# Kernel tuning notes

Measured on AMD Instinct MI355X. Metric: run time of the kernel, lower is better.

## Reference

```python
import jax, jax.numpy as jnp
import numpy as np

B, TIN, IN, TRI, D, FFN, L, OUT = 8, 1040, 80, 128, 512, 2048, 8, 1024
H, DH, STRIDE, SEG, RC, LC, MAXMEM = 8, 64, 4, 16, 4, 32, 4
NEG = -1e8
SCALE = DH ** -0.5


def _layer_norm(x, g, b, eps=1e-5):
    m = jnp.mean(x, -1, keepdims=True)
    v = jnp.var(x, -1, keepdims=True)
    return (x - m) * jax.lax.rsqrt(v + eps) * g + b


def _build_attention_mask(U, nseg):
    # Faithful port of Emformer._gen_attention_mask; True = masked out.
    rct = RC * nseg
    mlen = nseg - 1
    rc_rows, q_rows, s_rows = [], [], []
    for i in range(nseg):
        rs, re = i * RC, i * RC + RC
        ss, se = max(i * SEG - LC, 0), min((i + 1) * SEG, U)
        ms = max(i - MAXMEM, 0)
        widths = [ms, i - ms, mlen - i, rs, RC, rct - re, ss, se - ss, U - se]

        def row(allowed):
            return np.concatenate([np.full(max(w, 0), j in allowed, dtype=bool)
                                   for j, w in enumerate(widths)])

        r = row({1, 4, 7})  # memory, own rc block, own (left-extended) segment
        rc_rows.append(np.tile(r, (RC, 1)))
        q_rows.append(np.tile(r, (min(SEG, U - i * SEG), 1)))
        s_rows.append(row({4, 7})[None])  # summary: rc block + segment only
    allow = np.concatenate([np.concatenate(rc_rows), np.concatenate(q_rows), np.concatenate(s_rows)])
    return jnp.asarray(~allow)


def _forward(input, lengths, w_in, ln_in_g, ln_in_b, wq, bq, wk, bk, wv, bv, wo, bo,
             ff_ln_g, ff_ln_b, w1, b1, w2, b2, ln_out_g, ln_out_b, w_out, b_out, lng, lnb):
    x = input @ w_in                                    # (B, TIN, TRI) input_linear (no bias)
    nb, t, _ = x.shape
    nf = t - t % STRIDE
    x = x[:, :nf].reshape(nb, nf // STRIDE, TRI * STRIDE)  # time reduction -> (B, Tr, D)
    lr = lengths // STRIDE
    x = jnp.transpose(x, (1, 0, 2))                     # (Tr, B, D) time-major like torch Emformer
    Tr = x.shape[0]
    U = Tr - RC                                         # utterance length (256)
    nseg = -(-U // SEG)
    utt = x[:U]
    # right-context blocks: hard-copied per segment (last block = trailing rc)
    starts = np.concatenate([np.arange(1, nseg) * SEG, [Tr - RC]])
    idx = (starts[:, None] + np.arange(RC)[None, :]).reshape(-1)
    rc = x[idx]                                         # (nseg*RC, B, D)
    Rt = rc.shape[0]
    Q = Rt + U + nseg                                   # rc + utterance + summary queries
    K = (nseg - 1) + Rt + U                             # mems + rc + utterance keys
    attn_mask = _build_attention_mask(U, nseg)          # (Q, K)
    mems0 = utt.reshape(nseg, SEG, nb, D).mean(1)[:-1]  # AvgPool1d(seg) on raw utterance, drop last
    # padding mask over keys (faithful to _gen_padding_mask)
    rcbl = Q - jnp.max(lr) - nseg
    klen = lr + (nseg - 1) + rcbl
    pad = jnp.arange(K)[None, :] >= klen[:, None]       # (B, K), True = masked

    def step(carry, p):
        utt, rc, mems = carry
        g1, be1, Wq, Bq, Wk, Bk, Wv, Bv, Wo, Bo, g2, be2, Wf1, Bf1, Wf2, Bf2, g3, be3 = p
        ln = _layer_norm(jnp.concatenate([rc, utt]), g1, be1)
        ln_rc, ln_utt = ln[:Rt], ln[Rt:]
        summary = ln_utt.reshape(nseg, SEG, nb, D).mean(1)       # (nseg, B, D)
        qin = jnp.concatenate([ln_rc, ln_utt, summary])          # (Q, B, D)
        kin = jnp.concatenate([mems, ln_rc, ln_utt])             # (K, B, D)
        q = (qin @ Wq + Bq).reshape(Q, nb, H, DH)
        k = (kin @ Wk + Bk).reshape(K, nb, H, DH)
        v = (kin @ Wv + Bv).reshape(K, nb, H, DH)
        w = jnp.einsum('qbhd,kbhd->bhqk', q * SCALE, k)
        w = jnp.where(attn_mask[None, None], NEG, w)
        w = jnp.where(pad[:, None, None, :], NEG, w)
        probs = jax.nn.softmax(w, axis=-1)
        att = jnp.einsum('bhqk,kbhd->qbhd', probs, v).reshape(Q, nb, D)
        out = att @ Wo + Bo
        rcu = out[:Rt + U]
        new_mems = jnp.tanh(out[Rt + U:])[:-1]                   # tanh_on_mem=True, drop last summary
        res = rcu + jnp.concatenate([rc, utt])                   # residual w/ pre-LN input
        h = _layer_norm(res, g2, be2)
        h = jax.nn.relu(h @ Wf1 + Bf1) @ Wf2 + Bf2               # pos_ff (pre-LN inside)
        res = res + h
        res = _layer_norm(res, g3, be3)
        return (res[Rt:], res[:Rt], new_mems), None

    xs = (ln_in_g, ln_in_b, wq, bq, wk, bk, wv, bv, wo, bo,
          ff_ln_g, ff_ln_b, w1, b1, w2, b2, ln_out_g, ln_out_b)
    (utt, rc, mems), _ = jax.lax.scan(step, (utt, rc, mems0), xs)
    y = jnp.transpose(utt, (1, 0, 2))                   # (B, U, D)
    y = _layer_norm(y @ w_out + b_out, lng, lnb)        # output_linear + LayerNorm
    return y, lr


def setup_inputs() -> dict:
    key = jax.random.key(0)
    ks = jax.random.split(key, 12)

    def w(k, shape, fan):
        return jax.random.normal(k, shape, jnp.float32) / np.sqrt(fan)

    return {
        "input": jax.random.normal(ks[0], (B, TIN, IN), jnp.float32),
        "lengths": jax.random.randint(ks[1], (B,), 256, 1025, jnp.int32),
        "w_in": w(ks[2], (IN, TRI), IN),
        "ln_in_g": jnp.ones((L, D), jnp.float32), "ln_in_b": jnp.zeros((L, D), jnp.float32),
        "wq": w(ks[3], (L, D, D), D), "bq": jnp.zeros((L, D), jnp.float32),
        "wk": w(ks[4], (L, D, D), D), "bk": jnp.zeros((L, D), jnp.float32),
        "wv": w(ks[5], (L, D, D), D), "bv": jnp.zeros((L, D), jnp.float32),
        "wo": w(ks[6], (L, D, D), D), "bo": jnp.zeros((L, D), jnp.float32),
        "ff_ln_g": jnp.ones((L, D), jnp.float32), "ff_ln_b": jnp.zeros((L, D), jnp.float32),
        "w1": w(ks[7], (L, D, FFN), D), "b1": jnp.zeros((L, FFN), jnp.float32),
        "w2": w(ks[8], (L, FFN, D), FFN), "b2": jnp.zeros((L, D), jnp.float32),
        "ln_out_g": jnp.ones((L, D), jnp.float32), "ln_out_b": jnp.zeros((L, D), jnp.float32),
        "w_out": w(ks[9], (D, OUT), D), "b_out": jnp.zeros((OUT,), jnp.float32),
        "lng": jnp.ones((OUT,), jnp.float32), "lnb": jnp.zeros((OUT,), jnp.float32),
    }


def reference(input, lengths, w_in, ln_in_g, ln_in_b, wq, bq, wk, bk, wv, bv, wo, bo,
              ff_ln_g, ff_ln_b, w1, b1, w2, b2, ln_out_g, ln_out_b, w_out, b_out, lng, lnb):
    return _forward(input, lengths, w_in, ln_in_g, ln_in_b, wq, bq, wk, bk, wv, bv, wo, bo,
                    ff_ln_g, ff_ln_b, w1, b1, w2, b2, ln_out_g, ln_out_b, w_out, b_out, lng, lnb)
```

## Files before the change

kernel.cpp:

```cpp
#include <hip/hip_runtime.h>
#include <math.h>

#define NB 8
#define D 512
#define H 8
#define DH 64
#define NSEG 16
#define RT 64
#define UU 256
#define QN 336
#define KN 335
#define SROWS 320
#define FFN_D 2048
#define LAYERS 8
#define OUTD 1024
#define TR 260
#define NEGV (-100000000.0f)
#define QSCALE 0.125f

typedef __attribute__((ext_vector_type(8))) short bf16x8;
typedef __attribute__((ext_vector_type(4))) float f32x4;

__device__ inline unsigned short f2bf(float f) {
    union { float f; unsigned int u; } v; v.f = f;
    unsigned int u = v.u;
    unsigned int r = (u + 0x7FFFu + ((u >> 16) & 1u)) >> 16;
    return (unsigned short)r;
}
__device__ inline float bf2f(unsigned short h) {
    union { unsigned int u; float f; } v; v.u = ((unsigned int)h) << 16;
    return v.f;
}

__device__ inline void async16(const void* g, void* l) {
    __builtin_amdgcn_global_load_lds((const __attribute__((address_space(1))) void*)g,
                                     (__attribute__((address_space(3))) void*)l, 16, 0, 0);
}

__global__ void lr_k(const int* __restrict__ lengths, int* __restrict__ lrw,
                     float* __restrict__ out_lr) {
    if (threadIdx.x == 0) {
        int mx = 0;
        for (int b = 0; b < NB; ++b) {
            int v = lengths[b] >> 2;
            lrw[b] = v;
            out_lr[b] = (float)v;
            if (v > mx) mx = v;
        }
        lrw[NB] = mx;
    }
}

__global__ __launch_bounds__(128) void inproj_k(const float* __restrict__ input,
                                                const float* __restrict__ w_in,
                                                float* __restrict__ XB) {
    __shared__ float wl[80 * 128];
    __shared__ float il[4 * 80];
    int tid = threadIdx.x;
    int t = blockIdx.x >> 3;
    int b = blockIdx.x & 7;
    for (int i = tid; i < 80 * 128; i += 128) wl[i] = w_in[i];
    const float* inp = input + ((size_t)b * 1040 + (size_t)t * 4) * 80;
    for (int i = tid; i < 320; i += 128) il[i] = inp[i];
    __syncthreads();
    float* xrow = XB + ((size_t)(t * NB + b)) * D;
#pragma unroll
    for (int c = 0; c < 4; ++c) {
        float acc = 0.f;
        for (int i = 0; i < 80; ++i) acc = fmaf(il[c * 80 + i], wl[i * 128 + tid], acc);
        xrow[c * 128 + tid] = acc;
    }
}

__global__ __launch_bounds__(256) void initstate_k(const float* __restrict__ XB,
                                                   float* __restrict__ S) {
    int r = blockIdx.x;
    int srow = r >> 3, b = r & 7;
    int src;
    if (srow < RT) {
        int i = srow >> 2, jj = srow & 3;
        src = (i < 15 ? (i + 1) * 16 : 256) + jj;
    } else {
        src = srow - RT;
    }
    const float* xr = XB + ((size_t)(src * NB + b)) * D;
    float* sr = S + (size_t)r * D;
    sr[threadIdx.x] = xr[threadIdx.x];
    sr[threadIdx.x + 256] = xr[threadIdx.x + 256];
}

__global__ __launch_bounds__(256) void mems0_k(const float* __restrict__ XB,
                                               unsigned short* __restrict__ MEMS) {
    int ib = blockIdx.x;
    int i = ib >> 3, b = ib & 7;
    for (int c = 0; c < 2; ++c) {
        int col = threadIdx.x + c * 256;
        float s = 0.f;
#pragma unroll
        for (int t = 0; t < 16; ++t) s += XB[((size_t)((i * 16 + t) * NB + b)) * D + col];
        MEMS[(size_t)ib * D + col] = f2bf(s * (1.f / 16.f));
    }
}

__global__ __launch_bounds__(256) void ln2_k(float* __restrict__ X,
                                             unsigned short* __restrict__ Y16,
                                             const float* __restrict__ gA,
                                             const float* __restrict__ bA,
                                             const float* __restrict__ gB,
                                             const float* __restrict__ bB, int fused) {
    int row = blockIdx.x;
    float* x = X + (size_t)row * D;
    __shared__ float rs_[4], rss_[4], rs2[4], rss2[4];
    int w = threadIdx.x >> 6;
    float v[2];
    float s = 0.f, ss = 0.f;
#pragma unroll
    for (int j = 0; j < 2; ++j) {
        v[j] = x[threadIdx.x + j * 256];
        s += v[j];
        ss = fmaf(v[j], v[j], ss);
    }
#pragma unroll
    for (int off = 32; off; off >>= 1) {
        s += __shfl_xor(s, off);
        ss += __shfl_xor(ss, off);
    }
    if ((threadIdx.x & 63) == 0) { rs_[w] = s; rss_[w] = ss; }
    __syncthreads();
    s = rs_[0] + rs_[1] + rs_[2] + rs_[3];
    ss = rss_[0] + rss_[1] + rss_[2] + rss_[3];
    float mean = s * (1.f / D);
    float var = ss * (1.f / D) - mean * mean;
    float rstd = rsqrtf(var + 1e-5f);
    float y1[2];
#pragma unroll
    for (int j = 0; j < 2; ++j) {
        int col = threadIdx.x + j * 256;
        y1[j] = (v[j] - mean) * rstd * gA[col] + bA[col];
    }
    if (!fused) {
#pragma unroll
        for (int j = 0; j < 2; ++j)
            Y16[(size_t)row * D + threadIdx.x + j * 256] = f2bf(y1[j]);
        return;
    }
    float s2 = 0.f, ss2 = 0.f;
#pragma unroll
    for (int j = 0; j < 2; ++j) {
        s2 += y1[j];
        ss2 = fmaf(y1[j], y1[j], ss2);
    }
#pragma unroll
    for (int off = 32; off; off >>= 1) {
        s2 += __shfl_xor(s2, off);
        ss2 += __shfl_xor(ss2, off);
    }
    if ((threadIdx.x & 63) == 0) { rs2[w] = s2; rss2[w] = ss2; }
    __syncthreads();
    s2 = rs2[0] + rs2[1] + rs2[2] + rs2[3];
    ss2 = rss2[0] + rss2[1] + rss2[2] + rss2[3];
    float mean2 = s2 * (1.f / D);
    float var2 = ss2 * (1.f / D) - mean2 * mean2;
    float rstd2 = rsqrtf(var2 + 1e-5f);
#pragma unroll
    for (int j = 0; j < 2; ++j) {
        int col = threadIdx.x + j * 256;
        x[col] = y1[j];
        Y16[(size_t)row * D + col] = f2bf((y1[j] - mean2) * rstd2 * gB[col] + bB[col]);
    }
}

__global__ __launch_bounds__(256) void ln_res_k(const float* __restrict__ OUTB,
                                                float* __restrict__ SB,
                                                unsigned short* __restrict__ MEMS,
                                                unsigned short* __restrict__ Y16,
                                                const float* __restrict__ g,
                                                const float* __restrict__ be) {
    int row = blockIdx.x;
    if (row >= SROWS * NB) {
        int j = row - SROWS * NB;
#pragma unroll
        for (int c = 0; c < 2; ++c) {
            int col = threadIdx.x + c * 256;
            MEMS[(size_t)j * D + col] = f2bf(tanhf(OUTB[(size_t)row * D + col]));
        }
        return;
    }
    float v[2];
    float s = 0.f, ss = 0.f;
#pragma unroll
    for (int j = 0; j < 2; ++j) {
        int col = threadIdx.x + j * 256;
        float r = SB[(size_t)row * D + col] + OUTB[(size_t)row * D + col];
        SB[(size_t)row * D + col] = r;
        v[j] = r;
        s += r;
        ss = fmaf(r, r, ss);
    }
#pragma unroll
    for (int off = 32; off; off >>= 1) {
        s += __shfl_xor(s, off);
        ss += __shfl_xor(ss, off);
    }
    __shared__ float rs_[4], rss_[4];
    int w = threadIdx.x >> 6;
    if ((threadIdx.x & 63) == 0) {
        rs_[w] = s;
        rss_[w] = ss;
    }
    __syncthreads();
    s = rs_[0] + rs_[1] + rs_[2] + rs_[3];
    ss = rss_[0] + rss_[1] + rss_[2] + rss_[3];
    float mean = s * (1.f / D);
    float var = ss * (1.f / D) - mean * mean;
    float rstd = rsqrtf(var + 1e-5f);
#pragma unroll
    for (int j = 0; j < 2; ++j) {
        int col = threadIdx.x + j * 256;
        Y16[(size_t)row * D + col] = f2bf((v[j] - mean) * rstd * g[col] + be[col]);
    }
}

__global__ __launch_bounds__(256) void summary_k(const unsigned short* __restrict__ LN16,
                                                 unsigned short* __restrict__ SUM16) {
    int ib = blockIdx.x;
    int i = ib >> 3, b = ib & 7;
    for (int c = 0; c < 2; ++c) {
        int col = threadIdx.x + c * 256;
        float s = 0.f;
#pragma unroll
        for (int t = 0; t < 16; ++t)
            s += bf2f(LN16[((size_t)((RT + i * 16 + t) * NB + b)) * D + col]);
        SUM16[(size_t)ib * D + col] = f2bf(s * (1.f / 16.f));
    }
}

__device__ inline void conv_tile64(float (*tile)[65], const float* __restrict__ src, int srcN,
                                   int k0, int sn0, unsigned short* __restrict__ dst, int dstK,
                                   int dn0) {
    int t = threadIdx.x;
#pragma unroll
    for (int p = 0; p < 4; ++p) {
        int r = p * 16 + (t >> 4);
        int c = (t & 15) * 4;
        *(float4*)&tile[r][c] = *(const float4*)&src[(size_t)(k0 + r) * srcN + sn0 + c];
    }
    __syncthreads();
#pragma unroll
    for (int p = 0; p < 2; ++p) {
        int rn = p * 32 + (t >> 3);
        int kc = (t & 7) * 8;
        int4 o;
        o.x = (int)f2bf(tile[kc + 0][rn]) | ((int)f2bf(tile[kc + 1][rn]) << 16);
        o.y = (int)f2bf(tile[kc + 2][rn]) | ((int)f2bf(tile[kc + 3][rn]) << 16);
        o.z = (int)f2bf(tile[kc + 4][rn]) | ((int)f2bf(tile[kc + 5][rn]) << 16);
        o.w = (int)f2bf(tile[kc + 6][rn]) | ((int)f2bf(tile[kc + 7][rn]) << 16);
        *(int4*)&dst[(size_t)(dn0 + rn) * dstK + k0 + kc] = o;
    }
    __syncthreads();
}

__global__ __launch_bounds__(256) void convw_all_k(const float* __restrict__ wq,
                                                   const float* __restrict__ wk,
                                                   const float* __restrict__ wv,
                                                   const float* __restrict__ wo,
                                                   const float* __restrict__ w1,
                                                   const float* __restrict__ w2,
                                                   const float* __restrict__ bq,
                                                   const float* __restrict__ bk,
                                                   const float* __restrict__ bv,
                                                   const float* __restrict__ w_out,
                                                   unsigned short* __restrict__ WQKV,
                                                   unsigned short* __restrict__ WO16,
                                                   unsigned short* __restrict__ W1T,
                                                   unsigned short* __restrict__ W2T,
                                                   unsigned short* __restrict__ WOUT16,
                                                   float* __restrict__ BQKV) {
    __shared__ float tile[64][65];
    int tb = blockIdx.x;
    if (tb >= LAYERS * 768) {
        int t = tb - LAYERS * 768;
        int n0 = (t % 16) * 64, k0 = (t / 16) * 64;
        conv_tile64(tile, w_out, 1024, k0, n0, WOUT16, 512, n0);
        return;
    }
    int l = tb / 768, t = tb % 768;
    if (t == 0) {
        for (int i = threadIdx.x; i < 1536; i += 256)
            BQKV[l * 1536 + i] = i < 512 ? bq[l * 512 + i]
                                         : (i < 1024 ? bk[l * 512 + i - 512]
                                                     : bv[l * 512 + i - 1024]);
    }
    if (t < 192) {
        int n0 = (t % 24) * 64, k0 = (t / 24) * 64;
        const float* src;
        int sn0;
        if (n0 < 512) { src = wq + (size_t)l * 262144; sn0 = n0; }
        else if (n0 < 1024) { src = wk + (size_t)l * 262144; sn0 = n0 - 512; }
        else { src = wv + (size_t)l * 262144; sn0 = n0 - 1024; }
        conv_tile64(tile, src, 512, k0, sn0, WQKV + (size_t)l * 1536 * 512, 512, n0);
    } else if (t < 256) {
        int tt = t - 192;
        int n0 = (tt % 8) * 64, k0 = (tt / 8) * 64;
        conv_tile64(tile, wo + (size_t)l * 262144, 512, k0, n0, WO16 + (size_t)l * 512 * 512, 512,
                    n0);
    } else if (t < 512) {
        int tt = t - 256;
        int n0 = (tt % 32) * 64, k0 = (tt / 32) * 64;
        conv_tile64(tile, w1 + (size_t)l * 1048576, 2048, k0, n0, W1T + (size_t)l * 2048 * 512,
                    512, n0);
    } else {
        int tt = t - 512;
        int n0 = (tt % 8) * 64, k0 = (tt / 8) * 64;
        conv_tile64(tile, w2 + (size_t)l * 1048576, 512, k0, n0, W2T + (size_t)l * 512 * 2048,
                    2048, n0);
    }
}

template <int BK>
__global__ __launch_bounds__(256) void gemm16_k(const unsigned short* __restrict__ A,
                                                const unsigned short* __restrict__ BT,
                                                const float* __restrict__ bias,
                                                void* __restrict__ Cp, int M, int N, int K,
                                                int Kchunk, int flags) {
    constexpr int CH = BK / 8;
    constexpr int NQ = CH / 4;
    __shared__ unsigned short As[64 * BK];
    __shared__ unsigned short Bs[64 * BK];
    int tid = threadIdx.x;
    int wave = tid >> 6, lane = tid & 63;
    int wm = wave >> 1, wn = wave & 1;
    int quad = lane >> 4, sub = lane & 15;
    int m0 = blockIdx.y * 64, n0 = blockIdx.x * 64;
    int kb = blockIdx.z * Kchunk;

    const unsigned short* gA[NQ];
    const unsigned short* gB[NQ];
    unsigned short* lA[NQ];
    unsigned short* lB[NQ];
#pragma unroll
    for (int q = 0; q < NQ; ++q) {
        int s = wave * (64 * NQ) + q * 64 + lane;
        int r = s / CH;
        int c = (s % CH) ^ (r & (CH - 1));
        int gra = m0 + r;
        if (gra >= M) gra = M - 1;
        gA[q] = A + (size_t)gra * K + kb + c * 8;
        gB[q] = BT + (size_t)(n0 + r) * K + kb + c * 8;
        lA[q] = &As[(wave * (64 * NQ) + q * 64) * 8];
        lB[q] = &Bs[(wave * (64 * NQ) + q * 64) * 8];
    }

    int rowA0 = wm * 32 + sub, rowA1 = rowA0 + 16;
    int rowB0 = wn * 32 + sub, rowB1 = rowB0 + 16;

    f32x4 acc[2][2] = {};
    for (int k0 = 0; k0 < Kchunk; k0 += BK) {
#pragma unroll
        for (int q = 0; q < NQ; ++q) {
            async16(gA[q] + k0, lA[q]);
            async16(gB[q] + k0, lB[q]);
        }
        __syncthreads();
#pragma unroll
        for (int ks = 0; ks < BK / 32; ++ks) {
            int cc = ks * 4 + quad;
            bf16x8 af0 = *(const bf16x8*)&As[rowA0 * BK + ((cc ^ (rowA0 & (CH - 1))) * 8)];
            bf16x8 af1 = *(const bf16x8*)&As[rowA1 * BK + ((cc ^ (rowA1 & (CH - 1))) * 8)];
            bf16x8 bf0 = *(const bf16x8*)&Bs[rowB0 * BK + ((cc ^ (rowB0 & (CH - 1))) * 8)];
            bf16x8 bf1 = *(const bf16x8*)&Bs[rowB1 * BK + ((cc ^ (rowB1 & (CH - 1))) * 8)];
            acc[0][0] = __builtin_amdgcn_mfma_f32_16x16x32_bf16(af0, bf0, acc[0][0], 0, 0, 0);
            acc[0][1] = __builtin_amdgcn_mfma_f32_16x16x32_bf16(af0, bf1, acc[0][1], 0, 0, 0);
            acc[1][0] = __builtin_amdgcn_mfma_f32_16x16x32_bf16(af1, bf0, acc[1][0], 0, 0, 0);
            acc[1][1] = __builtin_amdgcn_mfma_f32_16x16x32_bf16(af1, bf1, acc[1][1], 0, 0, 0);
        }
        __syncthreads();
    }

    bool relu = flags & 1, addc = flags & 2, obf = flags & 4, atom = flags & 8;
    bool addbias = !atom || blockIdx.z == 0;
    float* Cf = (float*)Cp;
    unsigned short* Ch = (unsigned short*)Cp;
#pragma unroll
    for (int mi = 0; mi < 2; ++mi) {
#pragma unroll
        for (int ni = 0; ni < 2; ++ni) {
#pragma unroll
            for (int r = 0; r < 4; ++r) {
                int row = m0 + wm * 32 + mi * 16 + quad * 4 + r;
                int col = n0 + wn * 32 + ni * 16 + sub;
                if (row < M) {
                    float v = acc[mi][ni][r] + (addbias ? bias[col] : 0.f);
                    if (relu) v = fmaxf(v, 0.f);
                    size_t idx = (size_t)row * N + col;
                    if (obf) {
                        Ch[idx] = f2bf(v);
                    } else if (atom) {
                        atomicAdd(&Cf[idx], v);
                    } else {
                        if (addc) v += Cf[idx];
                        Cf[idx] = v;
                    }
                }
            }
        }
    }
}

__global__ __launch_bounds__(256) void attn_k(const unsigned short* __restrict__ QKV,
                                              unsigned short* __restrict__ ATT,
                                              const int* __restrict__ lrw) {
    int tid = threadIdx.x;
    int qrow = blockIdx.x;
    int b = blockIdx.y;

    int i, is_sum;
    if (qrow < RT) {
        i = qrow >> 2;
        is_sum = 0;
    } else if (qrow < RT + UU) {
        i = (qrow - RT) >> 4;
        is_sum = 0;
    } else {
        i = qrow - (RT + UU);
        is_sum = 1;
    }
    int ms = (i > 4) ? (i - 4) : 0;
    int n_mem = is_sum ? 0 : (i - ms);
    int us = (i * 16 - 32 > 0) ? (i * 16 - 32) : 0;
    int ue = (i + 1) * 16;
    int total = n_mem + 4 + (ue - us);
    int klen = KN + lrw[b] - lrw[NB];

    __shared__ float qs[512];
    __shared__ float sc[H][64];
    __shared__ int kks[64];

    {
        const unsigned int* qrp =
            (const unsigned int*)&QKV[(size_t)(120 + qrow * NB + b) * 1536];
        unsigned int u = qrp[tid];
        qs[2 * tid] = __uint_as_float(u << 16) * QSCALE;
        qs[2 * tid + 1] = __uint_as_float(u & 0xFFFF0000u) * QSCALE;
    }
    if (tid < 64) {
        int kk = -1;
        if (tid < total) {
            if (tid < n_mem)
                kk = ms + tid;
            else if (tid < n_mem + 4)
                kk = 15 + i * 4 + (tid - n_mem);
            else
                kk = 79 + us + (tid - n_mem - 4);
        }
        kks[tid] = kk;
    }
    __syncthreads();

#pragma unroll
    for (int rep = 0; rep < 2; ++rep) {
        int p = rep * 256 + tid;
        int h = p >> 6, j = p & 63;
        int kk = kks[j];
        float s = NEGV;
        if (kk >= 0 && kk < klen) {
            const int4* kr = (const int4*)&QKV[(size_t)(kk * NB + b) * 1536 + 512 + h * DH];
            const float* qh = &qs[h * DH];
            float accd = 0.f;
#pragma unroll
            for (int c = 0; c < 8; ++c) {
                int4 kv = kr[c];
                const int uu[4] = {kv.x, kv.y, kv.z, kv.w};
#pragma unroll
                for (int jj = 0; jj < 4; ++jj) {
                    float lo = __uint_as_float(((unsigned)uu[jj]) << 16);
                    float hi = __uint_as_float(((unsigned)uu[jj]) & 0xFFFF0000u);
                    accd = fmaf(lo, qh[c * 8 + jj * 2], accd);
                    accd = fmaf(hi, qh[c * 8 + jj * 2 + 1], accd);
                }
            }
            s = accd;
        }
        sc[h][j] = s;
    }
    __syncthreads();

    {
        int wv = tid >> 6, lane = tid & 63;
#pragma unroll
        for (int hh = 0; hh < 2; ++hh) {
            int h = wv + hh * 4;
            float s = sc[h][lane];
            float m = s;
#pragma unroll
            for (int off = 32; off; off >>= 1) m = fmaxf(m, __shfl_xor(m, off));
            float p = __expf(s - m);
            float sum = p;
#pragma unroll
            for (int off = 32; off; off >>= 1) sum += __shfl_xor(sum, off);
            sc[h][lane] = p / sum;
        }
    }
    __syncthreads();

    {
        int h = tid >> 5;
        const float* ph = sc[h];
        float a0 = 0.f, a1 = 0.f;
        const unsigned short* vbase = QKV + (size_t)b * 1536 + 1024 + 2 * tid;
#pragma unroll 4
        for (int j = 0; j < total; ++j) {
            int kkj = kks[j];
            unsigned int u = *(const unsigned int*)&vbase[(size_t)kkj * (NB * 1536)];
            float p = ph[j];
            a0 = fmaf(p, __uint_as_float(u << 16), a0);
            a1 = fmaf(p, __uint_as_float(u & 0xFFFF0000u), a1);
        }
        unsigned int o = ((unsigned int)f2bf(a0)) | (((unsigned int)f2bf(a1)) << 16);
        *(unsigned int*)&ATT[(size_t)(qrow * NB + b) * D + 2 * tid] = o;
    }
}

__global__ __launch_bounds__(256) void final_ln_k(const float* __restrict__ Yb,
                                                  const float* __restrict__ g,
                                                  const float* __restrict__ be,
                                                  float* __restrict__ out) {
    int row = blockIdx.x;
    int u = row >> 3, b = row & 7;
    const float* x = Yb + (size_t)row * OUTD;
    float v[4];
    float s = 0.f, ss = 0.f;
#pragma unroll
    for (int j = 0; j < 4; ++j) {
        v[j] = x[threadIdx.x + j * 256];
        s += v[j];
        ss = fmaf(v[j], v[j], ss);
    }
#pragma unroll
    for (int off = 32; off; off >>= 1) {
        s += __shfl_xor(s, off);
        ss += __shfl_xor(ss, off);
    }
    __shared__ float rs_[4], rss_[4];
    int w = threadIdx.x >> 6;
    if ((threadIdx.x & 63) == 0) {
        rs_[w] = s;
        rss_[w] = ss;
    }
    __syncthreads();
    s = rs_[0] + rs_[1] + rs_[2] + rs_[3];
    ss = rss_[0] + rss_[1] + rss_[2] + rss_[3];
    float mean = s * (1.f / OUTD);
    float var = ss * (1.f / OUTD) - mean * mean;
    float rstd = rsqrtf(var + 1e-5f);
    float* o = out + ((size_t)(b * 256 + u)) * OUTD;
#pragma unroll
    for (int j = 0; j < 4; ++j) {
        int col = threadIdx.x + j * 256;
        o[col] = (v[j] - mean) * rstd * g[col] + be[col];
    }
}

extern "C" void kernel_launch(void* const* d_in, const int* in_sizes, int n_in, void* d_out,
                              int out_size, void* d_ws, size_t ws_size, hipStream_t stream) {
    (void)in_sizes;
    (void)n_in;
    (void)out_size;
    (void)ws_size;
    const float* input = (const float*)d_in[0];
    const int* lengths = (const int*)d_in[1];
    const float* w_in = (const float*)d_in[2];
    const float* ln_in_g = (const float*)d_in[3];
    const float* ln_in_b = (const float*)d_in[4];
    const float* wq = (const float*)d_in[5];
    const float* bq = (const float*)d_in[6];
    const float* wk = (const float*)d_in[7];
    const float* bk = (const float*)d_in[8];
    const float* wv = (const float*)d_in[9];
    const float* bv = (const float*)d_in[10];
    const float* wo = (const float*)d_in[11];
    const float* bo = (const float*)d_in[12];
    const float* ff_g = (const float*)d_in[13];
    const float* ff_b = (const float*)d_in[14];
    const float* w1 = (const float*)d_in[15];
    const float* b1 = (const float*)d_in[16];
    const float* w2 = (const float*)d_in[17];
    const float* b2 = (const float*)d_in[18];
    const float* lo_g = (const float*)d_in[19];
    const float* lo_b = (const float*)d_in[20];
    const float* w_out = (const float*)d_in[21];
    const float* b_out = (const float*)d_in[22];
    const float* lng = (const float*)d_in[23];
    const float* lnb = (const float*)d_in[24];
    float* out = (float*)d_out;

    char* wsc = (char*)d_ws;
    size_t off = 0;
    auto alloc = [&](size_t bytes) {
        char* p = wsc + off;
        off += (bytes + 255) & ~(size_t)255;
        return p;
    };
    unsigned short* ACT16 = (unsigned short*)alloc(2816ULL * 512 * 2);
    unsigned short* ATT16 = (unsigned short*)alloc(2688ULL * 512 * 2);
    unsigned short* HB16 = (unsigned short*)alloc(2560ULL * 2048 * 2);
    unsigned short* QKVB = (unsigned short*)alloc(2816ULL * 1536 * 2);
    float* SB = (float*)alloc(2560ULL * 512 * 4);
    unsigned short* WQKV16 = (unsigned short*)alloc(8ULL * 1536 * 512 * 2);
    unsigned short* WO16 = (unsigned short*)alloc(8ULL * 512 * 512 * 2);
    unsigned short* W1T = (unsigned short*)alloc(8ULL * 2048 * 512 * 2);
    unsigned short* W2T = (unsigned short*)alloc(8ULL * 512 * 2048 * 2);
    unsigned short* WOUT16 = (unsigned short*)alloc(1024ULL * 512 * 2);
    float* BQKV = (float*)alloc(8ULL * 1536 * 4);
    int* LRW = (int*)alloc(64);

    unsigned short* MEMS16 = ACT16;
    unsigned short* LNB16 = ACT16 + 120 * 512;
    unsigned short* SUMB16 = ACT16 + 2680 * 512;
    float* XB = (float*)QKVB;
    float* OUTB = (float*)QKVB;
    float* HBf = (float*)QKVB;

    lr_k<<<1, 64, 0, stream>>>(lengths, LRW, out + (size_t)NB * 256 * 1024);
    convw_all_k<<<LAYERS * 768 + 128, 256, 0, stream>>>(wq, wk, wv, wo, w1, w2, bq, bk, bv,
                                                        w_out, WQKV16, WO16, W1T, W2T, WOUT16,
                                                        BQKV);
    inproj_k<<<TR * NB, 128, 0, stream>>>(input, w_in, XB);
    initstate_k<<<SROWS * NB, 256, 0, stream>>>(XB, SB);
    mems0_k<<<15 * NB, 256, 0, stream>>>(XB, MEMS16);

    for (int l = 0; l < LAYERS; ++l) {
        if (l == 0) {
            ln2_k<<<SROWS * NB, 256, 0, stream>>>(SB, LNB16, ln_in_g, ln_in_b, nullptr, nullptr,
                                                  0);
        } else {
            ln2_k<<<SROWS * NB, 256, 0, stream>>>(SB, LNB16, lo_g + (l - 1) * D,
                                                  lo_b + (l - 1) * D, ln_in_g + l * D,
                                                  ln_in_b + l * D, 1);
        }
        summary_k<<<NSEG * NB, 256, 0, stream>>>(LNB16, SUMB16);
        gemm16_k<128><<<dim3(24, 44, 1), 256, 0, stream>>>(
            ACT16, WQKV16 + (size_t)l * 1536 * 512, BQKV + l * 1536, QKVB, 2808, 1536, 512, 512,
            4);
        attn_k<<<dim3(QN, NB), 256, 0, stream>>>(QKVB, ATT16, LRW);
        gemm16_k<128><<<dim3(8, 42, 1), 256, 0, stream>>>(ATT16, WO16 + (size_t)l * 512 * 512,
                                                          bo + l * D, OUTB, QN * NB, D, D, 512,
                                                          0);
        ln_res_k<<<(SROWS + 15) * NB, 256, 0, stream>>>(OUTB, SB, MEMS16, LNB16, ff_g + l * D,
                                                        ff_b + l * D);
        gemm16_k<128><<<dim3(32, 40, 1), 256, 0, stream>>>(LNB16, W1T + (size_t)l * 2048 * 512,
                                                           b1 + l * FFN_D, HB16, SROWS * NB,
                                                           FFN_D, 512, 512, 1 | 4);
        gemm16_k<128><<<dim3(8, 40, 4), 256, 0, stream>>>(HB16, W2T + (size_t)l * 512 * 2048,
                                                          b2 + l * D, SB, SROWS * NB, D, FFN_D,
                                                          512, 8);
    }
    ln2_k<<<SROWS * NB, 256, 0, stream>>>(SB, LNB16, lo_g + 7 * D, lo_b + 7 * D, nullptr,
                                          nullptr, 0);
    gemm16_k<128><<<dim3(16, 32, 1), 256, 0, stream>>>(LNB16 + (size_t)RT * NB * D, WOUT16,
                                                       b_out, HBf, UU * NB, OUTD, 512, 512, 0);
    final_ln_k<<<UU * NB, 256, 0, stream>>>(HBf, lng, lnb, out);
}
```

Before: 1.170 ms.

## Double-buffer GEMM K-tiles and fold summary query into attention via linearity

The GEMM kernel now uses BK=64 with two LDS buffers, issuing async loads for the next K-tile while computing on the current one. This removes one barrier per iteration and overlaps global loads with MFMA work. Separately, the summary_k kernel is dropped. The summary query is computed inside attention as the mean of the projected queries of its 16 segment rows, which relies on the Q projection being linear. That shrinks the QKV GEMM by 128 rows and removes a launch, but the summary K/V rows it used to project are no longer computed, and rounding order changes slightly.

```diff
diff --git a/kernel.cpp b/kernel.cpp
--- a/kernel.cpp
+++ b/kernel.cpp
@@ -218,20 +218,6 @@
     for (int j = 0; j < 2; ++j) {
         int col = threadIdx.x + j * 256;
         Y16[(size_t)row * D + col] = f2bf((v[j] - mean) * rstd * g[col] + be[col]);
-    }
-}
-
-__global__ __launch_bounds__(256) void summary_k(const unsigned short* __restrict__ LN16,
-                                                 unsigned short* __restrict__ SUM16) {
-    int ib = blockIdx.x;
-    int i = ib >> 3, b = ib & 7;
-    for (int c = 0; c < 2; ++c) {
-        int col = threadIdx.x + c * 256;
-        float s = 0.f;
-#pragma unroll
-        for (int t = 0; t < 16; ++t)
-            s += bf2f(LN16[((size_t)((RT + i * 16 + t) * NB + b)) * D + col]);
-        SUM16[(size_t)ib * D + col] = f2bf(s * (1.f / 16.f));
     }
 }
 
@@ -317,16 +303,13 @@
     }
 }
 
-template <int BK>
 __global__ __launch_bounds__(256) void gemm16_k(const unsigned short* __restrict__ A,
                                                 const unsigned short* __restrict__ BT,
                                                 const float* __restrict__ bias,
                                                 void* __restrict__ Cp, int M, int N, int K,
                                                 int Kchunk, int flags) {
-    constexpr int CH = BK / 8;
-    constexpr int NQ = CH / 4;
-    __shared__ unsigned short As[64 * BK];
-    __shared__ unsigned short Bs[64 * BK];
+    __shared__ unsigned short As[2 * 64 * 64];
+    __shared__ unsigned short Bs[2 * 64 * 64];
     int tid = threadIdx.x;
     int wave = tid >> 6, lane = tid & 63;
     int wm = wave >> 1, wn = wave & 1;
@@ -334,47 +317,53 @@
     int m0 = blockIdx.y * 64, n0 = blockIdx.x * 64;
     int kb = blockIdx.z * Kchunk;
 
-    const unsigned short* gA[NQ];
-    const unsigned short* gB[NQ];
-    unsigned short* lA[NQ];
-    unsigned short* lB[NQ];
-#pragma unroll
-    for (int q = 0; q < NQ; ++q) {
-        int s = wave * (64 * NQ) + q * 64 + lane;
-        int r = s / CH;
-        int c = (s % CH) ^ (r & (CH - 1));
-        int gra = m0 + r;
-        if (gra >= M) gra = M - 1;
-        gA[q] = A + (size_t)gra * K + kb + c * 8;
-        gB[q] = BT + (size_t)(n0 + r) * K + kb + c * 8;
-        lA[q] = &As[(wave * (64 * NQ) + q * 64) * 8];
-        lB[q] = &Bs[(wave * (64 * NQ) + q * 64) * 8];
-    }
+    int s0 = wave * 128 + lane;
+    int s1 = s0 + 64;
+    int r0 = s0 >> 3, c0 = (s0 & 7) ^ (r0 & 7);
+    int r1 = s1 >> 3, c1 = (s1 & 7) ^ (r1 & 7);
+    int gra0 = m0 + r0; if (gra0 >= M) gra0 = M - 1;
+    int gra1 = m0 + r1; if (gra1 >= M) gra1 = M - 1;
+    const unsigned short* gA0 = A + (size_t)gra0 * K + kb + c0 * 8;
+    const unsigned short* gA1 = A + (size_t)gra1 * K + kb + c1 * 8;
+    const unsigned short* gB0 = BT + (size_t)(n0 + r0) * K + kb + c0 * 8;
+    const unsigned short* gB1 = BT + (size_t)(n0 + r1) * K + kb + c1 * 8;
+    int lo0 = (wave * 128) * 8;
+    int lo1 = (wave * 128 + 64) * 8;
 
     int rowA0 = wm * 32 + sub, rowA1 = rowA0 + 16;
     int rowB0 = wn * 32 + sub, rowB1 = rowB0 + 16;
 
+    int nIter = Kchunk >> 6;
     f32x4 acc[2][2] = {};
-    for (int k0 = 0; k0 < Kchunk; k0 += BK) {
-#pragma unroll
-        for (int q = 0; q < NQ; ++q) {
-            async16(gA[q] + k0, lA[q]);
-            async16(gB[q] + k0, lB[q]);
-        }
+
+    async16(gA0, &As[lo0]);
+    async16(gA1, &As[lo1]);
+    async16(gB0, &Bs[lo0]);
+    async16(gB1, &Bs[lo1]);
+
+    for (int it = 0; it < nIter; ++it) {
         __syncthreads();
-#pragma unroll
-        for (int ks = 0; ks < BK / 32; ++ks) {
+        int bo = (it & 1) * 4096;
+        if (it + 1 < nIter) {
+            int nb = ((it + 1) & 1) * 4096;
+            int ko = (it + 1) * 64;
+            async16(gA0 + ko, &As[nb + lo0]);
+            async16(gA1 + ko, &As[nb + lo1]);
+            async16(gB0 + ko, &Bs[nb + lo0]);
+            async16(gB1 + ko, &Bs[nb + lo1]);
+        }
+#pragma unroll
+        for (int ks = 0; ks < 2; ++ks) {
             int cc = ks * 4 + quad;
-            bf16x8 af0 = *(const bf16x8*)&As[rowA0 * BK + ((cc ^ (rowA0 & (CH - 1))) * 8)];
-            bf16x8 af1 = *(const bf16x8*)&As[rowA1 * BK + ((cc ^ (rowA1 & (CH - 1))) * 8)];
-            bf16x8 bf0 = *(const bf16x8*)&Bs[rowB0 * BK + ((cc ^ (rowB0 & (CH - 1))) * 8)];
-            bf16x8 bf1 = *(const bf16x8*)&Bs[rowB1 * BK + ((cc ^ (rowB1 & (CH - 1))) * 8)];
+            bf16x8 af0 = *(const bf16x8*)&As[bo + rowA0 * 64 + ((cc ^ (rowA0 & 7)) * 8)];
+            bf16x8 af1 = *(const bf16x8*)&As[bo + rowA1 * 64 + ((cc ^ (rowA1 & 7)) * 8)];
+            bf16x8 bf0 = *(const bf16x8*)&Bs[bo + rowB0 * 64 + ((cc ^ (rowB0 & 7)) * 8)];
+            bf16x8 bf1 = *(const bf16x8*)&Bs[bo + rowB1 * 64 + ((cc ^ (rowB1 & 7)) * 8)];
             acc[0][0] = __builtin_amdgcn_mfma_f32_16x16x32_bf16(af0, bf0, acc[0][0], 0, 0, 0);
             acc[0][1] = __builtin_amdgcn_mfma_f32_16x16x32_bf16(af0, bf1, acc[0][1], 0, 0, 0);
             acc[1][0] = __builtin_amdgcn_mfma_f32_16x16x32_bf16(af1, bf0, acc[1][0], 0, 0, 0);
             acc[1][1] = __builtin_amdgcn_mfma_f32_16x16x32_bf16(af1, bf1, acc[1][1], 0, 0, 0);
         }
-        __syncthreads();
     }
 
     bool relu = flags & 1, addc = flags & 2, obf = flags & 4, atom = flags & 8;
@@ -436,12 +425,24 @@
     __shared__ float sc[H][64];
     __shared__ int kks[64];
 
-    {
+    if (!is_sum) {
         const unsigned int* qrp =
             (const unsigned int*)&QKV[(size_t)(120 + qrow * NB + b) * 1536];
         unsigned int u = qrp[tid];
         qs[2 * tid] = __uint_as_float(u << 16) * QSCALE;
         qs[2 * tid + 1] = __uint_as_float(u & 0xFFFF0000u) * QSCALE;
+    } else {
+        const unsigned int* qrp =
+            (const unsigned int*)&QKV[(size_t)(120 + (RT + i * 16) * NB + b) * 1536];
+        float a0 = 0.f, a1 = 0.f;
+#pragma unroll
+        for (int t = 0; t < 16; ++t) {
+            unsigned int u = qrp[(size_t)t * (NB * 768) + tid];
+            a0 += __uint_as_float(u << 16);
+            a1 += __uint_as_float(u & 0xFFFF0000u);
+        }
+        qs[2 * tid] = a0 * (QSCALE / 16.f);
+        qs[2 * tid + 1] = a1 * (QSCALE / 16.f);
     }
     if (tid < 64) {
         int kk = -1;
@@ -601,10 +602,10 @@
         off += (bytes + 255) & ~(size_t)255;
         return p;
     };
-    unsigned short* ACT16 = (unsigned short*)alloc(2816ULL * 512 * 2);
+    unsigned short* ACT16 = (unsigned short*)alloc(2688ULL * 512 * 2);
     unsigned short* ATT16 = (unsigned short*)alloc(2688ULL * 512 * 2);
     unsigned short* HB16 = (unsigned short*)alloc(2560ULL * 2048 * 2);
-    unsigned short* QKVB = (unsigned short*)alloc(2816ULL * 1536 * 2);
+    unsigned short* QKVB = (unsigned short*)alloc(2688ULL * 1536 * 2);
     float* SB = (float*)alloc(2560ULL * 512 * 4);
     unsigned short* WQKV16 = (unsigned short*)alloc(8ULL * 1536 * 512 * 2);
     unsigned short* WO16 = (unsigned short*)alloc(8ULL * 512 * 512 * 2);
@@ -616,7 +617,6 @@
 
     unsigned short* MEMS16 = ACT16;
     unsigned short* LNB16 = ACT16 + 120 * 512;
-    unsigned short* SUMB16 = ACT16 + 2680 * 512;
     float* XB = (float*)QKVB;
     float* OUTB = (float*)QKVB;
     float* HBf = (float*)QKVB;
@@ -638,26 +638,24 @@
                                                   lo_b + (l - 1) * D, ln_in_g + l * D,
                                                   ln_in_b + l * D, 1);
         }
-        summary_k<<<NSEG * NB, 256, 0, stream>>>(LNB16, SUMB16);
-        gemm16_k<128><<<dim3(24, 44, 1), 256, 0, stream>>>(
-            ACT16, WQKV16 + (size_t)l * 1536 * 512, BQKV + l * 1536, QKVB, 2808, 1536, 512, 512,
-            4);
+        gemm16_k<<<dim3(24, 42, 1), 256, 0, stream>>>(ACT16, WQKV16 + (size_t)l * 1536 * 512,
+                                                      BQKV + l * 1536, QKVB, 2680, 1536, 512,
+                                                      512, 4);
         attn_k<<<dim3(QN, NB), 256, 0, stream>>>(QKVB, ATT16, LRW);
-        gemm16_k<128><<<dim3(8, 42, 1), 256, 0, stream>>>(ATT16, WO16 + (size_t)l * 512 * 512,
-                                                          bo + l * D, OUTB, QN * NB, D, D, 512,
-                                                          0);
+        gemm16_k<<<dim3(8, 42, 1), 256, 0, stream>>>(ATT16, WO16 + (size_t)l * 512 * 512,
+                                                     bo + l * D, OUTB, QN * NB, D, D, 512, 0);
         ln_res_k<<<(SROWS + 15) * NB, 256, 0, stream>>>(OUTB, SB, MEMS16, LNB16, ff_g + l * D,
                                                         ff_b + l * D);
-        gemm16_k<128><<<dim3(32, 40, 1), 256, 0, stream>>>(LNB16, W1T + (size_t)l * 2048 * 512,
-                                                           b1 + l * FFN_D, HB16, SROWS * NB,
-                                                           FFN_D, 512, 512, 1 | 4);
-        gemm16_k<128><<<dim3(8, 40, 4), 256, 0, stream>>>(HB16, W2T + (size_t)l * 512 * 2048,
-                                                          b2 + l * D, SB, SROWS * NB, D, FFN_D,
-                                                          512, 8);
+        gemm16_k<<<dim3(32, 40, 1), 256, 0, stream>>>(LNB16, W1T + (size_t)l * 2048 * 512,
+                                                      b1 + l * FFN_D, HB16, SROWS * NB, FFN_D,
+                                                      512, 512, 1 | 4);
+        gemm16_k<<<dim3(8, 40, 4), 256, 0, stream>>>(HB16, W2T + (size_t)l * 512 * 2048,
+                                                     b2 + l * D, SB, SROWS * NB, D, FFN_D, 512,
+                                                     8);
     }
     ln2_k<<<SROWS * NB, 256, 0, stream>>>(SB, LNB16, lo_g + 7 * D, lo_b + 7 * D, nullptr,
                                           nullptr, 0);
-    gemm16_k<128><<<dim3(16, 32, 1), 256, 0, stream>>>(LNB16 + (size_t)RT * NB * D, WOUT16,
-                                                       b_out, HBf, UU * NB, OUTD, 512, 512, 0);
+    gemm16_k<<<dim3(16, 32, 1), 256, 0, stream>>>(LNB16 + (size_t)RT * NB * D, WOUT16, b_out,
+                                                  HBf, UU * NB, OUTD, 512, 512, 0);
     final_ln_k<<<UU * NB, 256, 0, stream>>>(HBf, lng, lnb, out);
 }
```

Measured after the change: 1.176 ms. About the same (+0.5%).
